# Kernel optimization log

Measured on AMD Instinct MI355X. Metric: run time of the kernel, lower is better.

## Reference

```python
import jax, jax.numpy as jnp
import numpy as np

B, L, D = 8, 2048, 64


def setup_inputs() -> dict:
    key = jax.random.key(0)
    kq, kk, kv = jax.random.split(key, 3)
    query = jax.random.normal(kq, (B, L, D), dtype=jnp.float32)
    key_t = jax.random.normal(kk, (B, L, D), dtype=jnp.float32)
    value = jax.random.normal(kv, (B, L, D), dtype=jnp.float32)
    return {"query": query, "key": key_t, "value": value}


def reference(query, key, value):
    d = query.shape[-1]
    # e = Q K^T / sqrt(d_k)   -> [B, Lq, Lk]
    scale = 1.0 / np.sqrt(float(d)).astype(np.float32)
    e = jnp.einsum("bqd,bkd->bqk", query, key) * scale
    # stable softmax over keys (matches exp(e - max)/sum in source)
    attention = jax.nn.softmax(e, axis=-1)
    # v = A V   -> [B, Lq, Dv]
    return jnp.einsum("bqk,bkd->bqd", attention, value)
```

## Files before the change

### kernel.cpp

```cpp
#include <hip/hip_runtime.h>


#define B_ 8
#define L_ 2048
#define D_ 64
#define NT 256
#define TK 32

typedef _Float16 half8_t __attribute__((ext_vector_type(8)));
typedef _Float16 half4_t __attribute__((ext_vector_type(4)));
typedef float f32x4 __attribute__((ext_vector_type(4)));

#define SCALE_LOG2E 0.1803368801111244f

__global__ __launch_bounds__(NT) void prepass(
    const float* __restrict__ K, const float* __restrict__ V,
    _Float16* __restrict__ K16, _Float16* __restrict__ VT16)
{
    const int blk = blockIdx.x;
    const int t = threadIdx.x;
    if (blk < 512) {
        const int i = blk * NT + t;
        const float4* s4 = (const float4*)K;
        const float4 a = s4[2 * i], b = s4[2 * i + 1];
        half8_t w;
        w[0] = (_Float16)a.x; w[1] = (_Float16)a.y;
        w[2] = (_Float16)a.z; w[3] = (_Float16)a.w;
        w[4] = (_Float16)b.x; w[5] = (_Float16)b.y;
        w[6] = (_Float16)b.z; w[7] = (_Float16)b.w;
        ((half8_t*)K16)[i] = w;
    } else {
        __shared__ __align__(16) _Float16 Lt[64 * 72];
        const int vblk = blk - 512;
        const int bb = vblk >> 5;
        const int kt = vblk & 31;
        const int r  = t >> 2;
        const int ch = t & 3;
        const float* vrow = V + ((size_t)bb * L_ + kt * 64 + r) * D_ + ch * 16;
        #pragma unroll
        for (int i = 0; i < 4; ++i) {
            const float4 f = ((const float4*)vrow)[i];
            const int d0 = ch * 16 + i * 4;
            Lt[(d0 + 0) * 72 + r] = (_Float16)f.x;
            Lt[(d0 + 1) * 72 + r] = (_Float16)f.y;
            Lt[(d0 + 2) * 72 + r] = (_Float16)f.z;
            Lt[(d0 + 3) * 72 + r] = (_Float16)f.w;
        }
        __syncthreads();
        const int d  = t >> 2;
        const int c2 = t & 3;
        const half8_t w0 = *(const half8_t*)&Lt[d * 72 + c2 * 16];
        const half8_t w1 = *(const half8_t*)&Lt[d * 72 + c2 * 16 + 8];
        _Float16* orow = VT16 + ((size_t)bb * D_ + d) * L_ + kt * 64 + c2 * 16;
        *(half8_t*)orow = w0;
        *(half8_t*)(orow + 8) = w1;
    }
}


#define LOADK(KB, BK)                                                           \
    {                                                                           \
        _Pragma("unroll") for (int s = 0; s < 2; ++s)                           \
        _Pragma("unroll") for (int c = 0; c < 2; ++c)                           \
            BK[s][c] = *(const half8_t*)&Kb[(size_t)((KB) + s * 16 + l15) * D_ + c * 32 + quad * 8]; \
    }

#define PROC(KB, BK)                                                            \
    {                                                                           \
        half4_t av[4][2];                                                       \
        _Pragma("unroll") for (int d = 0; d < 4; ++d)                           \
        _Pragma("unroll") for (int ks = 0; ks < 2; ++ks)                        \
            av[d][ks] = *(const half4_t*)&Vb[(size_t)(d * 16 + l15) * L_ + (KB) + ks * 16 + quad * 4]; \
        f32x4 sc[2][4];                                                         \
        _Pragma("unroll") for (int ks = 0; ks < 2; ++ks)                        \
        _Pragma("unroll") for (int qs = 0; qs < 4; ++qs) {                      \
            f32x4 acc = (f32x4){0.f, 0.f, 0.f, 0.f};                            \
            acc = __builtin_amdgcn_mfma_f32_16x16x32_f16(BK[ks][0], bq[qs][0], acc, 0, 0, 0); \
            acc = __builtin_amdgcn_mfma_f32_16x16x32_f16(BK[ks][1], bq[qs][1], acc, 0, 0, 0); \
            sc[ks][qs] = acc;                                                   \
        }                                                                       \
        half4_t pb[2][4];                                                       \
        _Pragma("unroll") for (int ks = 0; ks < 2; ++ks)                        \
        _Pragma("unroll") for (int qs = 0; qs < 4; ++qs) {                      \
            const float p0 = __builtin_exp2f(sc[ks][qs][0]);                    \
            const float p1 = __builtin_exp2f(sc[ks][qs][1]);                    \
            const float p2 = __builtin_exp2f(sc[ks][qs][2]);                    \
            const float p3 = __builtin_exp2f(sc[ks][qs][3]);                    \
            lacc[qs] += (p0 + p1) + (p2 + p3);                                  \
            half4_t pv;                                                         \
            pv[0] = (_Float16)p0; pv[1] = (_Float16)p1;                         \
            pv[2] = (_Float16)p2; pv[3] = (_Float16)p3;                         \
            pb[ks][qs] = pv;                                                    \
        }                                                                       \
        _Pragma("unroll") for (int qs = 0; qs < 4; ++qs)                        \
        _Pragma("unroll") for (int d = 0; d < 4; ++d)                           \
        _Pragma("unroll") for (int ks = 0; ks < 2; ++ks)                        \
            ofr[qs][d] = __builtin_amdgcn_mfma_f32_16x16x16f16(av[d][ks], pb[ks][qs], ofr[qs][d], 0, 0, 0); \
    }

__global__ __launch_bounds__(NT) void attn_qs4(
    const float* __restrict__ Q,
    const _Float16* __restrict__ K16,
    const _Float16* __restrict__ VT16,
    float* __restrict__ O)
{
    __shared__ float Ored[256 * 33];
    __shared__ float Lred[256];

    const int t    = threadIdx.x;
    const int wave = t >> 6;
    const int lane = t & 63;
    const int quad = lane >> 4;
    const int l15  = lane & 15;

    const int b   = blockIdx.x & 7;
    const int qbi = blockIdx.x >> 3;
    const int qb  = qbi * 64;
    const int key0 = wave * (TK * 16);

    const _Float16* Kb = K16 + (size_t)b * L_ * D_;
    const _Float16* Vb = VT16 + (size_t)b * D_ * L_;

    half8_t bq[4][2];
    #pragma unroll
    for (int qs = 0; qs < 4; ++qs) {
        const float* qp = Q + ((size_t)b * L_ + qb + qs * 16 + l15) * D_ + quad * 8;
        #pragma unroll
        for (int c = 0; c < 2; ++c) {
            const float4 f0 = *(const float4*)(qp + c * 32);
            const float4 f1 = *(const float4*)(qp + c * 32 + 4);
            bq[qs][c][0] = (_Float16)(f0.x * SCALE_LOG2E);
            bq[qs][c][1] = (_Float16)(f0.y * SCALE_LOG2E);
            bq[qs][c][2] = (_Float16)(f0.z * SCALE_LOG2E);
            bq[qs][c][3] = (_Float16)(f0.w * SCALE_LOG2E);
            bq[qs][c][4] = (_Float16)(f1.x * SCALE_LOG2E);
            bq[qs][c][5] = (_Float16)(f1.y * SCALE_LOG2E);
            bq[qs][c][6] = (_Float16)(f1.z * SCALE_LOG2E);
            bq[qs][c][7] = (_Float16)(f1.w * SCALE_LOG2E);
        }
    }

    f32x4 ofr[4][4];
    #pragma unroll
    for (int qs = 0; qs < 4; ++qs)
        #pragma unroll
        for (int d = 0; d < 4; ++d)
            ofr[qs][d] = (f32x4){0.f, 0.f, 0.f, 0.f};
    float lacc[4] = {0.f, 0.f, 0.f, 0.f};

    half8_t bkA[2][2], bkB[2][2];
    LOADK(key0, bkA);
    for (int it = 0; it < 8; ++it) {
        const int kb = key0 + it * 64;
        LOADK(kb + 32, bkB);
        PROC(kb, bkA);
        LOADK(kb + 64, bkA);
        PROC(kb + 32, bkB);
    }

    #pragma unroll
    for (int qs = 0; qs < 4; ++qs) {
        float v = lacc[qs];
        v += __shfl_xor(v, 16, 64);
        v += __shfl_xor(v, 32, 64);
        lacc[qs] = v;
    }
    if (quad == 0) {
        #pragma unroll
        for (int qs = 0; qs < 4; ++qs)
            Lred[wave * 64 + qs * 16 + l15] = lacc[qs];
    }

    #pragma unroll
    for (int pass = 0; pass < 2; ++pass) {
        __syncthreads();
        #pragma unroll
        for (int qh = 0; qh < 2; ++qh) {
            const int qs = pass * 2 + qh;
            #pragma unroll
            for (int d = 0; d < 4; ++d)
                #pragma unroll
                for (int r = 0; r < 4; ++r)
                    Ored[(wave * 64 + lane) * 33 + qh * 16 + d * 4 + r] = ofr[qs][d][r];
        }
        __syncthreads();
        #pragma unroll
        for (int qh = 0; qh < 2; ++qh) {
            const int qs = pass * 2 + qh;
            const float lt = Lred[qs * 16 + l15] + Lred[64 + qs * 16 + l15]
                           + Lred[128 + qs * 16 + l15] + Lred[192 + qs * 16 + l15];
            const float inv = 1.0f / lt;
            f32x4 osum = (f32x4){0.f, 0.f, 0.f, 0.f};
            #pragma unroll
            for (int w2 = 0; w2 < 4; ++w2) {
                const float* src = &Ored[(w2 * 64 + lane) * 33 + qh * 16 + wave * 4];
                osum[0] += src[0]; osum[1] += src[1];
                osum[2] += src[2]; osum[3] += src[3];
            }
            float4 outv;
            outv.x = osum[0] * inv; outv.y = osum[1] * inv;
            outv.z = osum[2] * inv; outv.w = osum[3] * inv;
            *(float4*)&O[((size_t)b * L_ + qb + qs * 16 + l15) * D_ + wave * 16 + quad * 4] = outv;
        }
    }
}

#define KS 72
__global__ __launch_bounds__(NT) void attn_mfma_f16(
    const float* __restrict__ Q, const float* __restrict__ K,
    const float* __restrict__ V, float* __restrict__ O)
{
    __shared__ __align__(16) _Float16 Kt[64 * KS];
    __shared__ __align__(16) _Float16 Vt[D_ * KS];
    __shared__ __align__(16) _Float16 Pt[4][16 * KS];

    const int t = threadIdx.x;
    const int wave = t >> 6, lane = t & 63, quad = lane >> 4, l15 = lane & 15;
    const int bpb = L_ / 64;
    const int b = blockIdx.x / bpb;
    const int qb = (blockIdx.x % bpb) * 64 + wave * 16;
    const size_t boff = (size_t)b * L_ * D_;

    half8_t aq[2];
    {
        const float* qp = Q + boff + (size_t)(qb + l15) * D_ + quad * 8;
        #pragma unroll
        for (int c = 0; c < 2; ++c) {
            const float4* p4 = (const float4*)(qp + c * 32);
            const float4 f0 = p4[0], f1 = p4[1];
            aq[c][0] = (_Float16)f0.x; aq[c][1] = (_Float16)f0.y;
            aq[c][2] = (_Float16)f0.z; aq[c][3] = (_Float16)f0.w;
            aq[c][4] = (_Float16)f1.x; aq[c][5] = (_Float16)f1.y;
            aq[c][6] = (_Float16)f1.z; aq[c][7] = (_Float16)f1.w;
        }
    }
    f32x4 ofr[4];
    #pragma unroll
    for (int d = 0; d < 4; ++d) ofr[d] = (f32x4){0.f, 0.f, 0.f, 0.f};
    float lacc[4] = {0.f, 0.f, 0.f, 0.f};
    const int skey = t & 63, sdg = t >> 6;
    _Float16* Pw = &Pt[wave][0];

    for (int kt = 0; kt < L_ / 64; ++kt) {
        __syncthreads();
        {
            const float4* kg4 = (const float4*)(K + boff + (size_t)(kt * 64 + skey) * D_ + sdg * 16);
            const float4 f0 = kg4[0], f1 = kg4[1], f2 = kg4[2], f3 = kg4[3];
            half8_t w0, w1;
            w0[0] = (_Float16)f0.x; w0[1] = (_Float16)f0.y;
            w0[2] = (_Float16)f0.z; w0[3] = (_Float16)f0.w;
            w0[4] = (_Float16)f1.x; w0[5] = (_Float16)f1.y;
            w0[6] = (_Float16)f1.z; w0[7] = (_Float16)f1.w;
            w1[0] = (_Float16)f2.x; w1[1] = (_Float16)f2.y;
            w1[2] = (_Float16)f2.z; w1[3] = (_Float16)f2.w;
            w1[4] = (_Float16)f3.x; w1[5] = (_Float16)f3.y;
            w1[6] = (_Float16)f3.z; w1[7] = (_Float16)f3.w;
            *(half8_t*)&Kt[skey * KS + sdg * 16] = w0;
            *(half8_t*)&Kt[skey * KS + sdg * 16 + 8] = w1;
        }
        {
            const float4* vg4 = (const float4*)(V + boff + (size_t)(kt * 64 + skey) * D_ + sdg * 16);
            #pragma unroll
            for (int i = 0; i < 4; ++i) {
                const float4 f = vg4[i];
                const int d0 = sdg * 16 + i * 4;
                Vt[(d0 + 0) * KS + skey] = (_Float16)f.x;
                Vt[(d0 + 1) * KS + skey] = (_Float16)f.y;
                Vt[(d0 + 2) * KS + skey] = (_Float16)f.z;
                Vt[(d0 + 3) * KS + skey] = (_Float16)f.w;
            }
        }
        __syncthreads();
        #pragma unroll
        for (int s = 0; s < 4; ++s) {
            const half8_t bk0 = *(const half8_t*)&Kt[(s * 16 + l15) * KS + quad * 8];
            const half8_t bk1 = *(const half8_t*)&Kt[(s * 16 + l15) * KS + 32 + quad * 8];
            f32x4 sc = (f32x4){0.f, 0.f, 0.f, 0.f};
            sc = __builtin_amdgcn_mfma_f32_16x16x32_f16(aq[0], bk0, sc, 0, 0, 0);
            sc = __builtin_amdgcn_mfma_f32_16x16x32_f16(aq[1], bk1, sc, 0, 0, 0);
            #pragma unroll
            for (int r = 0; r < 4; ++r) {
                const float p = __expf(sc[r] * 0.125f);
                lacc[r] += p;
                Pw[(quad * 4 + r) * KS + s * 16 + l15] = (_Float16)p;
            }
        }
        __syncthreads();
        #pragma unroll
        for (int c = 0; c < 2; ++c) {
            const half8_t ap = *(const half8_t*)&Pw[l15 * KS + c * 32 + quad * 8];
            #pragma unroll
            for (int d = 0; d < 4; ++d) {
                const half8_t bv = *(const half8_t*)&Vt[(d * 16 + l15) * KS + c * 32 + quad * 8];
                ofr[d] = __builtin_amdgcn_mfma_f32_16x16x32_f16(ap, bv, ofr[d], 0, 0, 0);
            }
        }
    }
    #pragma unroll
    for (int r = 0; r < 4; ++r) {
        float v = lacc[r];
        v += __shfl_xor(v, 1, 64);
        v += __shfl_xor(v, 2, 64);
        v += __shfl_xor(v, 4, 64);
        v += __shfl_xor(v, 8, 64);
        lacc[r] = v;
    }
    #pragma unroll
    for (int r = 0; r < 4; ++r) {
        const float inv = 1.0f / lacc[r];
        float* orow = O + boff + (size_t)(qb + quad * 4 + r) * D_ + l15;
        #pragma unroll
        for (int d = 0; d < 4; ++d) orow[d * 16] = ofr[d][r] * inv;
    }
}

extern "C" void kernel_launch(void* const* d_in, const int* in_sizes, int n_in,
                              void* d_out, int out_size, void* d_ws, size_t ws_size,
                              hipStream_t stream) {
    const float* Q = (const float*)d_in[0];
    const float* K = (const float*)d_in[1];
    const float* V = (const float*)d_in[2];
    float* O = (float*)d_out;

    if (ws_size >= (size_t)8 * 1024 * 1024) {
        _Float16* K16  = (_Float16*)d_ws;
        _Float16* VT16 = K16 + (size_t)B_ * L_ * D_;
        prepass<<<768, NT, 0, stream>>>(K, V, K16, VT16);
        attn_qs4<<<256, NT, 0, stream>>>(Q, K16, VT16, O);
    } else {
        attn_mfma_f16<<<256, NT, 0, stream>>>(Q, K, V, O);
    }
}
```

Baseline: 92.36 us.

## Split keys across eight waves per block and prefetch V fragments

```diff
diff --git a/kernel.cpp b/kernel.cpp
--- a/kernel.cpp
+++ b/kernel.cpp
@@ -65,12 +65,15 @@
             BK[s][c] = *(const half8_t*)&Kb[(size_t)((KB) + s * 16 + l15) * D_ + c * 32 + quad * 8]; \
     }
 
-#define PROC(KB, BK)                                                            \
+#define LOADV(KB, AV)                                                           \
     {                                                                           \
-        half4_t av[4][2];                                                       \
         _Pragma("unroll") for (int d = 0; d < 4; ++d)                           \
         _Pragma("unroll") for (int ks = 0; ks < 2; ++ks)                        \
-            av[d][ks] = *(const half4_t*)&Vb[(size_t)(d * 16 + l15) * L_ + (KB) + ks * 16 + quad * 4]; \
+            AV[d][ks] = *(const half4_t*)&Vb[(size_t)(d * 16 + l15) * L_ + (KB) + ks * 16 + quad * 4]; \
+    }
+
+#define PROC(BK, AV)                                                            \
+    {                                                                           \
         f32x4 sc[2][4];                                                         \
         _Pragma("unroll") for (int ks = 0; ks < 2; ++ks)                        \
         _Pragma("unroll") for (int qs = 0; qs < 4; ++qs) {                      \
@@ -95,17 +98,17 @@
         _Pragma("unroll") for (int qs = 0; qs < 4; ++qs)                        \
         _Pragma("unroll") for (int d = 0; d < 4; ++d)                           \
         _Pragma("unroll") for (int ks = 0; ks < 2; ++ks)                        \
-            ofr[qs][d] = __builtin_amdgcn_mfma_f32_16x16x16f16(av[d][ks], pb[ks][qs], ofr[qs][d], 0, 0, 0); \
-    }
-
-__global__ __launch_bounds__(NT) void attn_qs4(
+            ofr[qs][d] = __builtin_amdgcn_mfma_f32_16x16x16f16(AV[d][ks], pb[ks][qs], ofr[qs][d], 0, 0, 0); \
+    }
+
+__global__ __launch_bounds__(512, 2) void attn_w8(
     const float* __restrict__ Q,
     const _Float16* __restrict__ K16,
     const _Float16* __restrict__ VT16,
     float* __restrict__ O)
 {
-    __shared__ float Ored[256 * 33];
-    __shared__ float Lred[256];
+    __shared__ float Ored[512 * 17];
+    __shared__ float Lred[512];
 
     const int t    = threadIdx.x;
     const int wave = t >> 6;
@@ -116,7 +119,7 @@
     const int b   = blockIdx.x & 7;
     const int qbi = blockIdx.x >> 3;
     const int qb  = qbi * 64;
-    const int key0 = wave * (TK * 16);
+    const int key0 = wave * 256;
 
     const _Float16* Kb = K16 + (size_t)b * L_ * D_;
     const _Float16* Vb = VT16 + (size_t)b * D_ * L_;
@@ -149,13 +152,17 @@
     float lacc[4] = {0.f, 0.f, 0.f, 0.f};
 
     half8_t bkA[2][2], bkB[2][2];
+    half4_t avA[4][2], avB[4][2];
     LOADK(key0, bkA);
-    for (int it = 0; it < 8; ++it) {
+    LOADV(key0, avA);
+    for (int it = 0; it < 4; ++it) {
         const int kb = key0 + it * 64;
         LOADK(kb + 32, bkB);
-        PROC(kb, bkA);
+        LOADV(kb + 32, avB);
+        PROC(bkA, avA);
         LOADK(kb + 64, bkA);
-        PROC(kb + 32, bkB);
+        LOADV(kb + 64, avA);
+        PROC(bkB, avB);
     }
 
     #pragma unroll
@@ -172,28 +179,24 @@
     }
 
     #pragma unroll
-    for (int pass = 0; pass < 2; ++pass) {
-        __syncthreads();
-        #pragma unroll
-        for (int qh = 0; qh < 2; ++qh) {
-            const int qs = pass * 2 + qh;
-            #pragma unroll
-            for (int d = 0; d < 4; ++d)
-                #pragma unroll
-                for (int r = 0; r < 4; ++r)
-                    Ored[(wave * 64 + lane) * 33 + qh * 16 + d * 4 + r] = ofr[qs][d][r];
-        }
-        __syncthreads();
-        #pragma unroll
-        for (int qh = 0; qh < 2; ++qh) {
-            const int qs = pass * 2 + qh;
+    for (int qs = 0; qs < 4; ++qs) {
+        __syncthreads();
+        #pragma unroll
+        for (int d = 0; d < 4; ++d)
+            #pragma unroll
+            for (int r = 0; r < 4; ++r)
+                Ored[(wave * 64 + lane) * 17 + d * 4 + r] = ofr[qs][d][r];
+        __syncthreads();
+        if (wave < 4) {
             const float lt = Lred[qs * 16 + l15] + Lred[64 + qs * 16 + l15]
-                           + Lred[128 + qs * 16 + l15] + Lred[192 + qs * 16 + l15];
+                           + Lred[128 + qs * 16 + l15] + Lred[192 + qs * 16 + l15]
+                           + Lred[256 + qs * 16 + l15] + Lred[320 + qs * 16 + l15]
+                           + Lred[384 + qs * 16 + l15] + Lred[448 + qs * 16 + l15];
             const float inv = 1.0f / lt;
             f32x4 osum = (f32x4){0.f, 0.f, 0.f, 0.f};
             #pragma unroll
-            for (int w2 = 0; w2 < 4; ++w2) {
-                const float* src = &Ored[(w2 * 64 + lane) * 33 + qh * 16 + wave * 4];
+            for (int w2 = 0; w2 < 8; ++w2) {
+                const float* src = &Ored[(w2 * 64 + lane) * 17 + wave * 4];
                 osum[0] += src[0]; osum[1] += src[1];
                 osum[2] += src[2]; osum[3] += src[3];
             }
@@ -326,7 +329,7 @@
         _Float16* K16  = (_Float16*)d_ws;
         _Float16* VT16 = K16 + (size_t)B_ * L_ * D_;
         prepass<<<768, NT, 0, stream>>>(K, V, K16, VT16);
-        attn_qs4<<<256, NT, 0, stream>>>(Q, K16, VT16, O);
+        attn_w8<<<256, 512, 0, stream>>>(Q, K16, VT16, O);
     } else {
         attn_mfma_f16<<<256, NT, 0, stream>>>(Q, K, V, O);
     }
```

Measured after the change: 93.94 us. About the same (+1.7%).

## Split attention block into 16 waves across query halves and key eighths

Applied to the files above, without the earlier changes.

```diff
diff --git a/kernel.cpp b/kernel.cpp
--- a/kernel.cpp
+++ b/kernel.cpp
@@ -5,7 +5,6 @@
 #define L_ 2048
 #define D_ 64
 #define NT 256
-#define TK 32
 
 typedef _Float16 half8_t __attribute__((ext_vector_type(8)));
 typedef _Float16 half4_t __attribute__((ext_vector_type(4)));
@@ -57,73 +56,34 @@
     }
 }
 
-
-#define LOADK(KB, BK)                                                           \
-    {                                                                           \
-        _Pragma("unroll") for (int s = 0; s < 2; ++s)                           \
-        _Pragma("unroll") for (int c = 0; c < 2; ++c)                           \
-            BK[s][c] = *(const half8_t*)&Kb[(size_t)((KB) + s * 16 + l15) * D_ + c * 32 + quad * 8]; \
-    }
-
-#define PROC(KB, BK)                                                            \
-    {                                                                           \
-        half4_t av[4][2];                                                       \
-        _Pragma("unroll") for (int d = 0; d < 4; ++d)                           \
-        _Pragma("unroll") for (int ks = 0; ks < 2; ++ks)                        \
-            av[d][ks] = *(const half4_t*)&Vb[(size_t)(d * 16 + l15) * L_ + (KB) + ks * 16 + quad * 4]; \
-        f32x4 sc[2][4];                                                         \
-        _Pragma("unroll") for (int ks = 0; ks < 2; ++ks)                        \
-        _Pragma("unroll") for (int qs = 0; qs < 4; ++qs) {                      \
-            f32x4 acc = (f32x4){0.f, 0.f, 0.f, 0.f};                            \
-            acc = __builtin_amdgcn_mfma_f32_16x16x32_f16(BK[ks][0], bq[qs][0], acc, 0, 0, 0); \
-            acc = __builtin_amdgcn_mfma_f32_16x16x32_f16(BK[ks][1], bq[qs][1], acc, 0, 0, 0); \
-            sc[ks][qs] = acc;                                                   \
-        }                                                                       \
-        half4_t pb[2][4];                                                       \
-        _Pragma("unroll") for (int ks = 0; ks < 2; ++ks)                        \
-        _Pragma("unroll") for (int qs = 0; qs < 4; ++qs) {                      \
-            const float p0 = __builtin_exp2f(sc[ks][qs][0]);                    \
-            const float p1 = __builtin_exp2f(sc[ks][qs][1]);                    \
-            const float p2 = __builtin_exp2f(sc[ks][qs][2]);                    \
-            const float p3 = __builtin_exp2f(sc[ks][qs][3]);                    \
-            lacc[qs] += (p0 + p1) + (p2 + p3);                                  \
-            half4_t pv;                                                         \
-            pv[0] = (_Float16)p0; pv[1] = (_Float16)p1;                         \
-            pv[2] = (_Float16)p2; pv[3] = (_Float16)p3;                         \
-            pb[ks][qs] = pv;                                                    \
-        }                                                                       \
-        _Pragma("unroll") for (int qs = 0; qs < 4; ++qs)                        \
-        _Pragma("unroll") for (int d = 0; d < 4; ++d)                           \
-        _Pragma("unroll") for (int ks = 0; ks < 2; ++ks)                        \
-            ofr[qs][d] = __builtin_amdgcn_mfma_f32_16x16x16f16(av[d][ks], pb[ks][qs], ofr[qs][d], 0, 0, 0); \
-    }
-
-__global__ __launch_bounds__(NT) void attn_qs4(
+__global__ __launch_bounds__(1024) void attn_hi(
     const float* __restrict__ Q,
     const _Float16* __restrict__ K16,
     const _Float16* __restrict__ VT16,
     float* __restrict__ O)
 {
-    __shared__ float Ored[256 * 33];
-    __shared__ float Lred[256];
+    __shared__ float Ored[512 * 17];
+    __shared__ float Lred[512];
 
     const int t    = threadIdx.x;
     const int wave = t >> 6;
     const int lane = t & 63;
     const int quad = lane >> 4;
     const int l15  = lane & 15;
+    const int qw   = wave >> 3;
+    const int kw   = wave & 7;
 
     const int b   = blockIdx.x & 7;
     const int qbi = blockIdx.x >> 3;
-    const int qb  = qbi * 64;
-    const int key0 = wave * (TK * 16);
+    const int qb  = qbi * 64 + qw * 32;
+    const int key0 = kw * 256;
 
     const _Float16* Kb = K16 + (size_t)b * L_ * D_;
     const _Float16* Vb = VT16 + (size_t)b * D_ * L_;
 
-    half8_t bq[4][2];
-    #pragma unroll
-    for (int qs = 0; qs < 4; ++qs) {
+    half8_t bq[2][2];
+    #pragma unroll
+    for (int qs = 0; qs < 2; ++qs) {
         const float* qp = Q + ((size_t)b * L_ + qb + qs * 16 + l15) * D_ + quad * 8;
         #pragma unroll
         for (int c = 0; c < 2; ++c) {
@@ -140,69 +100,110 @@
         }
     }
 
-    f32x4 ofr[4][4];
-    #pragma unroll
-    for (int qs = 0; qs < 4; ++qs)
+    f32x4 ofr[2][4];
+    #pragma unroll
+    for (int qs = 0; qs < 2; ++qs)
         #pragma unroll
         for (int d = 0; d < 4; ++d)
             ofr[qs][d] = (f32x4){0.f, 0.f, 0.f, 0.f};
-    float lacc[4] = {0.f, 0.f, 0.f, 0.f};
-
-    half8_t bkA[2][2], bkB[2][2];
-    LOADK(key0, bkA);
+    float lacc[2] = {0.f, 0.f};
+
     for (int it = 0; it < 8; ++it) {
-        const int kb = key0 + it * 64;
-        LOADK(kb + 32, bkB);
-        PROC(kb, bkA);
-        LOADK(kb + 64, bkA);
-        PROC(kb + 32, bkB);
-    }
-
-    #pragma unroll
-    for (int qs = 0; qs < 4; ++qs) {
+        const int kb = key0 + it * 32;
+
+        half8_t bk[2][2];
+        #pragma unroll
+        for (int s = 0; s < 2; ++s)
+            #pragma unroll
+            for (int c = 0; c < 2; ++c)
+                bk[s][c] = *(const half8_t*)&Kb[(size_t)(kb + s * 16 + l15) * D_ + c * 32 + quad * 8];
+        half4_t av[4][2];
+        #pragma unroll
+        for (int d = 0; d < 4; ++d)
+            #pragma unroll
+            for (int ks = 0; ks < 2; ++ks)
+                av[d][ks] = *(const half4_t*)&Vb[(size_t)(d * 16 + l15) * L_ + kb + ks * 16 + quad * 4];
+
+        f32x4 sc[2][2];
+        #pragma unroll
+        for (int ks = 0; ks < 2; ++ks)
+            #pragma unroll
+            for (int qs = 0; qs < 2; ++qs) {
+                f32x4 acc = (f32x4){0.f, 0.f, 0.f, 0.f};
+                acc = __builtin_amdgcn_mfma_f32_16x16x32_f16(bk[ks][0], bq[qs][0], acc, 0, 0, 0);
+                acc = __builtin_amdgcn_mfma_f32_16x16x32_f16(bk[ks][1], bq[qs][1], acc, 0, 0, 0);
+                sc[ks][qs] = acc;
+            }
+
+        half4_t pb[2][2];
+        #pragma unroll
+        for (int ks = 0; ks < 2; ++ks)
+            #pragma unroll
+            for (int qs = 0; qs < 2; ++qs) {
+                const float p0 = __builtin_exp2f(sc[ks][qs][0]);
+                const float p1 = __builtin_exp2f(sc[ks][qs][1]);
+                const float p2 = __builtin_exp2f(sc[ks][qs][2]);
+                const float p3 = __builtin_exp2f(sc[ks][qs][3]);
+                lacc[qs] += (p0 + p1) + (p2 + p3);
+                half4_t pv;
+                pv[0] = (_Float16)p0; pv[1] = (_Float16)p1;
+                pv[2] = (_Float16)p2; pv[3] = (_Float16)p3;
+                pb[ks][qs] = pv;
+            }
+
+        #pragma unroll
+        for (int qs = 0; qs < 2; ++qs)
+            #pragma unroll
+            for (int d = 0; d < 4; ++d)
+                #pragma unroll
+                for (int ks = 0; ks < 2; ++ks)
+                    ofr[qs][d] = __builtin_amdgcn_mfma_f32_16x16x16f16(av[d][ks], pb[ks][qs], ofr[qs][d], 0, 0, 0);
+    }
+
+    #pragma unroll
+    for (int qs = 0; qs < 2; ++qs) {
         float v = lacc[qs];
         v += __shfl_xor(v, 16, 64);
         v += __shfl_xor(v, 32, 64);
         lacc[qs] = v;
     }
     if (quad == 0) {
-        #pragma unroll
-        for (int qs = 0; qs < 4; ++qs)
-            Lred[wave * 64 + qs * 16 + l15] = lacc[qs];
-    }
-
-    #pragma unroll
-    for (int pass = 0; pass < 2; ++pass) {
-        __syncthreads();
-        #pragma unroll
-        for (int qh = 0; qh < 2; ++qh) {
-            const int qs = pass * 2 + qh;
-            #pragma unroll
-            for (int d = 0; d < 4; ++d)
+        Lred[wave * 32 + l15] = lacc[0];
+        Lred[wave * 32 + 16 + l15] = lacc[1];
+    }
+
+    #pragma unroll
+    for (int p = 0; p < 2; ++p)
+        #pragma unroll
+        for (int qs = 0; qs < 2; ++qs) {
+            __syncthreads();
+            if (qw == p) {
                 #pragma unroll
-                for (int r = 0; r < 4; ++r)
-                    Ored[(wave * 64 + lane) * 33 + qh * 16 + d * 4 + r] = ofr[qs][d][r];
-        }
-        __syncthreads();
-        #pragma unroll
-        for (int qh = 0; qh < 2; ++qh) {
-            const int qs = pass * 2 + qh;
-            const float lt = Lred[qs * 16 + l15] + Lred[64 + qs * 16 + l15]
-                           + Lred[128 + qs * 16 + l15] + Lred[192 + qs * 16 + l15];
-            const float inv = 1.0f / lt;
-            f32x4 osum = (f32x4){0.f, 0.f, 0.f, 0.f};
-            #pragma unroll
-            for (int w2 = 0; w2 < 4; ++w2) {
-                const float* src = &Ored[(w2 * 64 + lane) * 33 + qh * 16 + wave * 4];
-                osum[0] += src[0]; osum[1] += src[1];
-                osum[2] += src[2]; osum[3] += src[3];
-            }
-            float4 outv;
-            outv.x = osum[0] * inv; outv.y = osum[1] * inv;
-            outv.z = osum[2] * inv; outv.w = osum[3] * inv;
-            *(float4*)&O[((size_t)b * L_ + qb + qs * 16 + l15) * D_ + wave * 16 + quad * 4] = outv;
-        }
-    }
+                for (int d = 0; d < 4; ++d)
+                    #pragma unroll
+                    for (int r = 0; r < 4; ++r)
+                        Ored[(kw * 64 + lane) * 17 + d * 4 + r] = ofr[qs][d][r];
+            }
+            __syncthreads();
+            if (qw == p && kw < 4) {
+                float lt = 0.f;
+                #pragma unroll
+                for (int k2 = 0; k2 < 8; ++k2)
+                    lt += Lred[(p * 8 + k2) * 32 + qs * 16 + l15];
+                const float inv = 1.0f / lt;
+                f32x4 osum = (f32x4){0.f, 0.f, 0.f, 0.f};
+                #pragma unroll
+                for (int w2 = 0; w2 < 8; ++w2) {
+                    const float* src = &Ored[(w2 * 64 + lane) * 17 + kw * 4];
+                    osum[0] += src[0]; osum[1] += src[1];
+                    osum[2] += src[2]; osum[3] += src[3];
+                }
+                float4 outv;
+                outv.x = osum[0] * inv; outv.y = osum[1] * inv;
+                outv.z = osum[2] * inv; outv.w = osum[3] * inv;
+                *(float4*)&O[((size_t)b * L_ + qb + qs * 16 + l15) * D_ + kw * 16 + quad * 4] = outv;
+            }
+        }
 }
 
 #define KS 72
@@ -326,7 +327,7 @@
         _Float16* K16  = (_Float16*)d_ws;
         _Float16* VT16 = K16 + (size_t)B_ * L_ * D_;
         prepass<<<768, NT, 0, stream>>>(K, V, K16, VT16);
-        attn_qs4<<<256, NT, 0, stream>>>(Q, K16, VT16, O);
+        attn_hi<<<256, 1024, 0, stream>>>(Q, K16, VT16, O);
     } else {
         attn_mfma_f16<<<256, NT, 0, stream>>>(Q, K, V, O);
     }
```

After: 114.7 us. 24.2% more time.

## Pre-swizzle K and V into MFMA fragment order for contiguous per-lane loads

Applied to the files above, without the earlier changes.

```diff
diff --git a/kernel.cpp b/kernel.cpp
--- a/kernel.cpp
+++ b/kernel.cpp
@@ -5,7 +5,6 @@
 #define L_ 2048
 #define D_ 64
 #define NT 256
-#define TK 32
 
 typedef _Float16 half8_t __attribute__((ext_vector_type(8)));
 typedef _Float16 half4_t __attribute__((ext_vector_type(4)));
@@ -13,64 +12,69 @@
 
 #define SCALE_LOG2E 0.1803368801111244f
 
-__global__ __launch_bounds__(NT) void prepass(
+__global__ __launch_bounds__(NT) void prepass_frag(
     const float* __restrict__ K, const float* __restrict__ V,
-    _Float16* __restrict__ K16, _Float16* __restrict__ VT16)
+    _Float16* __restrict__ K16F, _Float16* __restrict__ VT16F)
 {
     const int blk = blockIdx.x;
     const int t = threadIdx.x;
     if (blk < 512) {
-        const int i = blk * NT + t;
-        const float4* s4 = (const float4*)K;
-        const float4 a = s4[2 * i], b = s4[2 * i + 1];
+        const int b  = blk >> 6;
+        const int kt = blk & 63;
+        const int p    = t >> 6;
+        const int lane = t & 63;
+        const int quad = lane >> 4;
+        const int l15  = lane & 15;
+        const int s = p >> 1, c = p & 1;
+        const int row = kt * 32 + s * 16 + l15;
+        const float* kp = K + ((size_t)b * L_ + row) * D_ + c * 32 + quad * 8;
+        const float4 f0 = *(const float4*)kp;
+        const float4 f1 = *(const float4*)(kp + 4);
         half8_t w;
-        w[0] = (_Float16)a.x; w[1] = (_Float16)a.y;
-        w[2] = (_Float16)a.z; w[3] = (_Float16)a.w;
-        w[4] = (_Float16)b.x; w[5] = (_Float16)b.y;
-        w[6] = (_Float16)b.z; w[7] = (_Float16)b.w;
-        ((half8_t*)K16)[i] = w;
+        w[0] = (_Float16)f0.x; w[1] = (_Float16)f0.y;
+        w[2] = (_Float16)f0.z; w[3] = (_Float16)f0.w;
+        w[4] = (_Float16)f1.x; w[5] = (_Float16)f1.y;
+        w[6] = (_Float16)f1.z; w[7] = (_Float16)f1.w;
+        *(half8_t*)&K16F[((size_t)(b * 64 + kt) * 4 + p) * 512 + lane * 8] = w;
     } else {
-        __shared__ __align__(16) _Float16 Lt[64 * 72];
-        const int vblk = blk - 512;
-        const int bb = vblk >> 5;
-        const int kt = vblk & 31;
-        const int r  = t >> 2;
-        const int ch = t & 3;
-        const float* vrow = V + ((size_t)bb * L_ + kt * 64 + r) * D_ + ch * 16;
-        #pragma unroll
-        for (int i = 0; i < 4; ++i) {
-            const float4 f = ((const float4*)vrow)[i];
-            const int d0 = ch * 16 + i * 4;
-            Lt[(d0 + 0) * 72 + r] = (_Float16)f.x;
-            Lt[(d0 + 1) * 72 + r] = (_Float16)f.y;
-            Lt[(d0 + 2) * 72 + r] = (_Float16)f.z;
-            Lt[(d0 + 3) * 72 + r] = (_Float16)f.w;
-        }
-        __syncthreads();
-        const int d  = t >> 2;
-        const int c2 = t & 3;
-        const half8_t w0 = *(const half8_t*)&Lt[d * 72 + c2 * 16];
-        const half8_t w1 = *(const half8_t*)&Lt[d * 72 + c2 * 16 + 8];
-        _Float16* orow = VT16 + ((size_t)bb * D_ + d) * L_ + kt * 64 + c2 * 16;
-        *(half8_t*)orow = w0;
-        *(half8_t*)(orow + 8) = w1;
+        const int vb = blk - 512;
+        const int b  = vb >> 6;
+        const int kt = vb & 63;
+        #pragma unroll
+        for (int i = 0; i < 2; ++i) {
+            const int slot = i * NT + t;
+            const int p    = slot >> 6;
+            const int lane = slot & 63;
+            const int quad = lane >> 4;
+            const int l15  = lane & 15;
+            const int d = p >> 1, ks = p & 1;
+            const int row = kt * 32 + ks * 16 + quad * 4;
+            const int col = d * 16 + l15;
+            const float* vp = V + ((size_t)b * L_ + row) * D_ + col;
+            half4_t a;
+            a[0] = (_Float16)vp[0];
+            a[1] = (_Float16)vp[D_];
+            a[2] = (_Float16)vp[2 * D_];
+            a[3] = (_Float16)vp[3 * D_];
+            *(half4_t*)&VT16F[((size_t)(b * 64 + kt) * 8 + p) * 256 + lane * 4] = a;
+        }
     }
 }
 
 
-#define LOADK(KB, BK)                                                           \
+#define LOADK(KT, BK)                                                           \
     {                                                                           \
         _Pragma("unroll") for (int s = 0; s < 2; ++s)                           \
         _Pragma("unroll") for (int c = 0; c < 2; ++c)                           \
-            BK[s][c] = *(const half8_t*)&Kb[(size_t)((KB) + s * 16 + l15) * D_ + c * 32 + quad * 8]; \
-    }
-
-#define PROC(KB, BK)                                                            \
+            BK[s][c] = *(const half8_t*)&KbF[((size_t)(KT) * 4 + s * 2 + c) * 512 + lane * 8]; \
+    }
+
+#define PROC(KT, BK)                                                            \
     {                                                                           \
         half4_t av[4][2];                                                       \
         _Pragma("unroll") for (int d = 0; d < 4; ++d)                           \
         _Pragma("unroll") for (int ks = 0; ks < 2; ++ks)                        \
-            av[d][ks] = *(const half4_t*)&Vb[(size_t)(d * 16 + l15) * L_ + (KB) + ks * 16 + quad * 4]; \
+            av[d][ks] = *(const half4_t*)&VbF[((size_t)(KT) * 8 + d * 2 + ks) * 256 + lane * 4]; \
         f32x4 sc[2][4];                                                         \
         _Pragma("unroll") for (int ks = 0; ks < 2; ++ks)                        \
         _Pragma("unroll") for (int qs = 0; qs < 4; ++qs) {                      \
@@ -98,10 +102,10 @@
             ofr[qs][d] = __builtin_amdgcn_mfma_f32_16x16x16f16(av[d][ks], pb[ks][qs], ofr[qs][d], 0, 0, 0); \
     }
 
-__global__ __launch_bounds__(NT) void attn_qs4(
+__global__ __launch_bounds__(NT) void attn_qs4f(
     const float* __restrict__ Q,
-    const _Float16* __restrict__ K16,
-    const _Float16* __restrict__ VT16,
+    const _Float16* __restrict__ K16F,
+    const _Float16* __restrict__ VT16F,
     float* __restrict__ O)
 {
     __shared__ float Ored[256 * 33];
@@ -116,10 +120,10 @@
     const int b   = blockIdx.x & 7;
     const int qbi = blockIdx.x >> 3;
     const int qb  = qbi * 64;
-    const int key0 = wave * (TK * 16);
-
-    const _Float16* Kb = K16 + (size_t)b * L_ * D_;
-    const _Float16* Vb = VT16 + (size_t)b * D_ * L_;
+    const int kt0 = wave * 16;
+
+    const _Float16* KbF = K16F + (size_t)b * 64 * 4 * 512;
+    const _Float16* VbF = VT16F + (size_t)b * 64 * 8 * 256;
 
     half8_t bq[4][2];
     #pragma unroll
@@ -149,13 +153,13 @@
     float lacc[4] = {0.f, 0.f, 0.f, 0.f};
 
     half8_t bkA[2][2], bkB[2][2];
-    LOADK(key0, bkA);
+    LOADK(kt0, bkA);
     for (int it = 0; it < 8; ++it) {
-        const int kb = key0 + it * 64;
-        LOADK(kb + 32, bkB);
-        PROC(kb, bkA);
-        LOADK(kb + 64, bkA);
-        PROC(kb + 32, bkB);
+        const int kta = kt0 + it * 2;
+        LOADK(kta + 1, bkB);
+        PROC(kta, bkA);
+        LOADK(kta + 2, bkA);
+        PROC(kta + 1, bkB);
     }
 
     #pragma unroll
@@ -323,10 +327,10 @@
     float* O = (float*)d_out;
 
     if (ws_size >= (size_t)8 * 1024 * 1024) {
-        _Float16* K16  = (_Float16*)d_ws;
-        _Float16* VT16 = K16 + (size_t)B_ * L_ * D_;
-        prepass<<<768, NT, 0, stream>>>(K, V, K16, VT16);
-        attn_qs4<<<256, NT, 0, stream>>>(Q, K16, VT16, O);
+        _Float16* K16F  = (_Float16*)d_ws;
+        _Float16* VT16F = K16F + (size_t)1048576;
+        prepass_frag<<<1024, NT, 0, stream>>>(K, V, K16F, VT16F);
+        attn_qs4f<<<256, NT, 0, stream>>>(Q, K16F, VT16F, O);
     } else {
         attn_mfma_f16<<<256, NT, 0, stream>>>(Q, K, V, O);
     }
```

Result: faster. 85.08 us (-7.9%).
